# Performance work log

Hardware: AMD Instinct MI355X
Metric: run time of the kernel (lower is better)

Reference implementation:

```python
import jax, jax.numpy as jnp
import numpy as np

B, C, H, W = 4, 64, 64, 64
CI = C // 4  # inter_channels for q/k convs and SE fc


def setup_inputs() -> dict:
    key = jax.random.key(0)
    ks = jax.random.split(key, 12)
    s = lambda k, shape, fan: jax.random.normal(k, shape, jnp.float32) * (1.0 / np.sqrt(fan))
    return {
        "ftr": jax.random.normal(ks[0], (B, C, H, W), jnp.float32),
        "wq": s(ks[1], (CI, C), C), "bq": jnp.zeros((CI,), jnp.float32),
        "wk": s(ks[2], (CI, C), C), "bk": jnp.zeros((CI,), jnp.float32),
        "wv": s(ks[3], (C, C), C),  "bv": jnp.zeros((C,), jnp.float32),
        "delta": jnp.array([0.1], jnp.float32),
        "w_avg1": s(ks[4], (CI, C), C), "w_avg2": s(ks[5], (C, CI), CI),
        "w_max1": s(ks[6], (CI, C), C), "w_max2": s(ks[7], (C, CI), CI),
    }


def reference(ftr, wq, bq, wk, bk, wv, bv, delta, w_avg1, w_avg2, w_max1, w_max2):
    b, c, h, w = ftr.shape
    p = h * w
    x = ftr.reshape(b, c, p)                                   # [B,C,P]
    q = jnp.einsum('oc,bcp->bpo', wq, x) + bq                  # [B,P,CI]
    k = jnp.einsum('oc,bcp->bop', wk, x) + bk[:, None]         # [B,CI,P]
    v = jnp.einsum('oc,bcp->bop', wv, x) + bv[:, None]         # [B,C,P]
    scores = jnp.einsum('bpo,boq->bpq', q, k)                  # [B,P,P]
    weights = jax.nn.softmax(scores, axis=1)                   # softmax over dim=1 (queries), as in torch code
    G = jnp.einsum('bcp,bpq->bcq', v, weights).reshape(b, c, h, w)
    out = delta[0] * G + ftr
    # ChannelRecalibration (SE with avg+max pooling)
    f_avg = jnp.mean(out, axis=(2, 3))                         # [B,C]
    f_max = jnp.max(out, axis=(2, 3))                          # [B,C]
    a = jax.nn.relu(f_avg @ w_avg1.T) @ w_avg2.T
    m = jax.nn.relu(f_max @ w_max1.T) @ w_max2.T
    gate = jax.nn.sigmoid(a + m)[:, :, None, None]
    return gate * out
```

## Files before the change

### kernel.cpp

```cpp
#include <hip/hip_runtime.h>
#include <math.h>

#define PP 4096

typedef __attribute__((ext_vector_type(8))) short short8;
typedef __attribute__((ext_vector_type(4))) short short4v;
typedef __attribute__((ext_vector_type(4))) float float4v;

__device__ __forceinline__ short f2bf(float f) {
    union { float f; unsigned u; } v; v.f = f;
    unsigned r = v.u + 0x7FFFu + ((v.u >> 16) & 1u);
    return (short)(r >> 16);
}

#if __has_builtin(__builtin_amdgcn_mfma_f32_16x16x16bf16_1k)
__device__ __forceinline__ float4v mfma16(short4v a, short4v b, float4v c) {
    return __builtin_amdgcn_mfma_f32_16x16x16bf16_1k(a, b, c, 0, 0, 0);
}
#else
__device__ __forceinline__ float4v mfma16(short4v a, short4v b, float4v c) {
    short8 a8 = {a[0], a[1], a[2], a[3], 0, 0, 0, 0};
    short8 b8 = {b[0], b[1], b[2], b[3], 0, 0, 0, 0};
    return __builtin_amdgcn_mfma_f32_16x16x32_bf16(a8, b8, c, 0, 0, 0);
}
#endif

__global__ __launch_bounds__(256) void qkv_kernel(
    const float* __restrict__ ftr, const float* __restrict__ wq, const float* __restrict__ bq,
    const float* __restrict__ wk, const float* __restrict__ bk,
    const float* __restrict__ wv, const float* __restrict__ bv,
    short* __restrict__ q16, short* __restrict__ k16, short* __restrict__ v_a)
{
    __shared__ float xs[64][68] __attribute__((aligned(16)));
    __shared__ float wvs[64][68] __attribute__((aligned(16)));
    __shared__ float wq_t[64][20] __attribute__((aligned(16)));
    __shared__ float wk_t[64][20] __attribute__((aligned(16)));

    const int b  = blockIdx.x >> 6;
    const int p0 = (blockIdx.x & 63) << 6;
    const int tid = threadIdx.x;

    for (int idx = tid; idx < 1024; idx += 256) {
        int c = idx >> 4, j4 = (idx & 15) << 2;
        *(float4*)&xs[c][j4] = *(const float4*)(ftr + ((size_t)(b * 64 + c)) * PP + p0 + j4);
    }
    for (int idx = tid; idx < 1024; idx += 256) {
        int r = idx >> 4, j4 = (idx & 15) << 2;
        *(float4*)&wvs[r][j4] = *(const float4*)(wv + r * 64 + j4);
    }
    for (int idx = tid; idx < 1024; idx += 256) {
        int o = idx >> 6, c2 = idx & 63;
        wq_t[c2][o] = wq[idx];
        wk_t[c2][o] = wk[idx];
    }
    __syncthreads();

    {
        const int wg = tid >> 6, qd = (tid >> 4) & 3, cc = tid & 15;
        const int c = wg * 16 + cc;
        const float bvc = bv[c];
        #pragma unroll
        for (int kt = 0; kt < 2; ++kt) {
            const int col = kt * 32 + qd * 8;
            float a[8] = {0.f,0.f,0.f,0.f,0.f,0.f,0.f,0.f};
            #pragma unroll 8
            for (int c2 = 0; c2 < 64; ++c2) {
                float w = wvs[c][c2];
                float4 xa = *(const float4*)&xs[c2][col];
                float4 xb = *(const float4*)&xs[c2][col + 4];
                a[0] += w * xa.x; a[1] += w * xa.y; a[2] += w * xa.z; a[3] += w * xa.w;
                a[4] += w * xb.x; a[5] += w * xb.y; a[6] += w * xb.z; a[7] += w * xb.w;
            }
            const int ptg = ((p0 + kt * 32) >> 4) + (qd >> 1);
            const int qp0 = (qd & 1) * 2;
            #pragma unroll
            for (int h = 0; h < 2; ++h) {
                short4v pv;
                #pragma unroll
                for (int j = 0; j < 4; ++j) pv[j] = f2bf(a[h * 4 + j] + bvc);
                *(short4v*)(v_a + ((((size_t)(b * 256 + ptg)) * 4 + wg) * 64 + (qp0 + h) * 16 + cc) * 4) = pv;
            }
        }
    }

    {
        const int p_l = tid >> 2, sel = tid & 3;
        const int half = sel & 1, arr = sel >> 1;
        const float* Wtr = arr ? &wk_t[0][0] : &wq_t[0][0];
        float a[8] = {0.f,0.f,0.f,0.f,0.f,0.f,0.f,0.f};
        #pragma unroll 8
        for (int c2 = 0; c2 < 64; ++c2) {
            float x = xs[c2][p_l];
            float4 wA = *(const float4*)(Wtr + c2 * 20 + half * 8);
            float4 wB = *(const float4*)(Wtr + c2 * 20 + half * 8 + 4);
            a[0] += wA.x * x; a[1] += wA.y * x; a[2] += wA.z * x; a[3] += wA.w * x;
            a[4] += wB.x * x; a[5] += wB.y * x; a[6] += wB.z * x; a[7] += wB.w * x;
        }
        const float* bias = arr ? bk : bq;
        const float scl = arr ? 1.0f : 1.4426950408889634f;
        short8 pq;
        #pragma unroll
        for (int oo = 0; oo < 8; ++oo)
            pq[oo] = f2bf((a[oo] + bias[half * 8 + oo]) * scl);
        short* dst = (arr ? k16 : q16) + (((size_t)(b * PP + p0 + p_l)) << 4) + half * 8;
        *(short8*)dst = pq;
    }
}

__global__ __launch_bounds__(512, 2) void attn_kernel(
    const short* __restrict__ q16, const short* __restrict__ k16,
    const short* __restrict__ v_a,
    const float* __restrict__ ftr, const float* __restrict__ delta,
    float* __restrict__ out, float* __restrict__ psum, float* __restrict__ pmax)
{
    __shared__ float Obuf[8][16][66];
    __shared__ float lb[8][64];
    __shared__ float lfin[64];

    const int b    = blockIdx.x >> 6;
    const int qblk = blockIdx.x & 63;
    const int q0   = qblk << 6;
    const int tid  = threadIdx.x;
    const int lane = tid & 63;
    const int n    = lane & 15;
    const int quad = lane >> 4;
    const int ph   = tid >> 6;

    const float4v zf4 = {0.f, 0.f, 0.f, 0.f};
    const short4v ones = {0x3F80, 0x3F80, 0x3F80, 0x3F80};

    short4v bkf[4];
    #pragma unroll
    for (int nt = 0; nt < 4; ++nt)
        bkf[nt] = *(const short4v*)(k16 + ((size_t)(b * PP + q0 + nt * 16 + n) << 4) + quad * 4);

    const short* qrow = q16 + ((size_t)(b * PP + n) << 4) + quad * 4;
    const short* vrow = v_a + (size_t)b * 262144 + lane * 4;

    float4v acc[4][4], lacc[4];
    #pragma unroll
    for (int mt = 0; mt < 4; ++mt)
        #pragma unroll
        for (int nt = 0; nt < 4; ++nt) acc[mt][nt] = zf4;
    #pragma unroll
    for (int nt = 0; nt < 4; ++nt) lacc[nt] = zf4;

    const int pt0 = ph * 512;
    for (int it = 0; it < 8; ++it) {
        const int pt = pt0 + it * 64;
        const int pti = pt >> 4;

        short4v aq[4];
        #pragma unroll
        for (int f = 0; f < 4; ++f)
            aq[f] = *(const short4v*)(qrow + (size_t)(pt + f * 16) * 16);
        short4v va[4][4];
        #pragma unroll
        for (int f = 0; f < 4; ++f)
            #pragma unroll
            for (int mt = 0; mt < 4; ++mt)
                va[f][mt] = *(const short4v*)(vrow + (size_t)((pti + f) * 4 + mt) * 256);

        float4v sf_c[4], sf_n[4];
        #pragma unroll
        for (int nt = 0; nt < 4; ++nt)
            sf_c[nt] = mfma16(aq[0], bkf[nt], zf4);

        #pragma unroll
        for (int f = 0; f < 4; ++f) {
            if (f < 3) {
                #pragma unroll
                for (int nt = 0; nt < 4; ++nt)
                    sf_n[nt] = mfma16(aq[f + 1], bkf[nt], zf4);
            }
            short4v w[4];
            #pragma unroll
            for (int nt = 0; nt < 4; ++nt) {
                float w0 = __builtin_amdgcn_exp2f(sf_c[nt][0]);
                float w1 = __builtin_amdgcn_exp2f(sf_c[nt][1]);
                float w2 = __builtin_amdgcn_exp2f(sf_c[nt][2]);
                float w3 = __builtin_amdgcn_exp2f(sf_c[nt][3]);
                union { uint2 u; short4v s; } cv;
                cv.u.x = __builtin_amdgcn_perm(__float_as_uint(w1), __float_as_uint(w0), 0x07060302u);
                cv.u.y = __builtin_amdgcn_perm(__float_as_uint(w3), __float_as_uint(w2), 0x07060302u);
                w[nt] = cv.s;
            }
            #pragma unroll
            for (int nt = 0; nt < 4; ++nt)
                lacc[nt] = mfma16(ones, w[nt], lacc[nt]);
            #pragma unroll
            for (int mt = 0; mt < 4; ++mt)
                #pragma unroll
                for (int nt = 0; nt < 4; ++nt)
                    acc[mt][nt] = mfma16(va[f][mt], w[nt], acc[mt][nt]);
            #pragma unroll
            for (int nt = 0; nt < 4; ++nt) sf_c[nt] = sf_n[nt];
        }
    }

    if (quad == 0) {
        #pragma unroll
        for (int nt = 0; nt < 4; ++nt)
            lb[ph][nt * 16 + n] = lacc[nt][0];
    }
    __syncthreads();
    if (tid < 64) {
        float s = 0.f;
        #pragma unroll
        for (int p8 = 0; p8 < 8; ++p8) s += lb[p8][tid];
        lfin[tid] = delta[0] / s;
    }
    __syncthreads();

    const int c_l = tid >> 5;
    const int q2  = (tid & 31) * 2;
    #pragma unroll
    for (int mt = 0; mt < 4; ++mt) {
        #pragma unroll
        for (int nt = 0; nt < 4; ++nt)
            #pragma unroll
            for (int i = 0; i < 4; ++i)
                Obuf[ph][quad * 4 + i][nt * 16 + n] = acc[mt][nt][i];
        __syncthreads();
        const int c = mt * 16 + c_l;
        float o0 = 0.f, o1 = 0.f;
        #pragma unroll
        for (int p8 = 0; p8 < 8; ++p8) {
            o0 += Obuf[p8][c_l][q2];
            o1 += Obuf[p8][c_l][q2 + 1];
        }
        const size_t g = ((size_t)(b * 64 + c)) * PP + q0 + q2;
        float2 fv = *(const float2*)(ftr + g);
        o0 = o0 * lfin[q2]     + fv.x;
        o1 = o1 * lfin[q2 + 1] + fv.y;
        float2 ov; ov.x = o0; ov.y = o1;
        *(float2*)(out + g) = ov;
        float s = o0 + o1, m = fmaxf(o0, o1);
        s += __shfl_xor(s, 1); s += __shfl_xor(s, 2);
        s += __shfl_xor(s, 4); s += __shfl_xor(s, 8); s += __shfl_xor(s, 16);
        m = fmaxf(m, __shfl_xor(m, 1)); m = fmaxf(m, __shfl_xor(m, 2));
        m = fmaxf(m, __shfl_xor(m, 4)); m = fmaxf(m, __shfl_xor(m, 8));
        m = fmaxf(m, __shfl_xor(m, 16));
        if ((tid & 31) == 0) {
            psum[((size_t)(b * 64) + qblk) * 64 + c] = s;
            pmax[((size_t)(b * 64) + qblk) * 64 + c] = m;
        }
        __syncthreads();
    }
}

__global__ __launch_bounds__(256) void reduce_gate_kernel(
    const float* __restrict__ psum, const float* __restrict__ pmax,
    const float* __restrict__ w_avg1, const float* __restrict__ w_avg2,
    const float* __restrict__ w_max1, const float* __restrict__ w_max2,
    float* __restrict__ gate)
{
    const int b = blockIdx.x, t = threadIdx.x;
    const int c = t & 63, ch = t >> 6;
    float s = 0.f, m = -3.4e38f;
    for (int i = 0; i < 16; ++i) {
        const int qb = ch * 16 + i;
        s += psum[((size_t)(b * 64) + qb) * 64 + c];
        m = fmaxf(m, pmax[((size_t)(b * 64) + qb) * 64 + c]);
    }
    __shared__ float ss[4][64], sm[4][64], fa[64], fm[64], ha[16], hm[16];
    ss[ch][c] = s; sm[ch][c] = m;
    __syncthreads();
    if (t < 64) {
        fa[t] = (ss[0][t] + ss[1][t] + ss[2][t] + ss[3][t]) * (1.f / 4096.f);
        fm[t] = fmaxf(fmaxf(sm[0][t], sm[1][t]), fmaxf(sm[2][t], sm[3][t]));
    }
    __syncthreads();
    if (t < 16) {
        float a = 0.f;
        for (int cc = 0; cc < 64; ++cc) a += fa[cc] * w_avg1[t * 64 + cc];
        ha[t] = fmaxf(a, 0.f);
    } else if (t < 32) {
        float a = 0.f;
        for (int cc = 0; cc < 64; ++cc) a += fm[cc] * w_max1[(t - 16) * 64 + cc];
        hm[t - 16] = fmaxf(a, 0.f);
    }
    __syncthreads();
    if (t < 64) {
        float a = 0.f, mm = 0.f;
        #pragma unroll
        for (int i = 0; i < 16; ++i) {
            a  += ha[i] * w_avg2[t * 16 + i];
            mm += hm[i] * w_max2[t * 16 + i];
        }
        gate[b * 64 + t] = 1.f / (1.f + expf(-(a + mm)));
    }
}

__global__ __launch_bounds__(256) void mul_kernel(
    float* __restrict__ out, const float* __restrict__ gate)
{
    const float g = gate[blockIdx.x >> 2];
    const size_t e = ((size_t)blockIdx.x * 256 + threadIdx.x) * 4;
    float4 v = *(const float4*)(out + e);
    v.x *= g; v.y *= g; v.z *= g; v.w *= g;
    *(float4*)(out + e) = v;
}

extern "C" void kernel_launch(void* const* d_in, const int* in_sizes, int n_in,
                              void* d_out, int out_size, void* d_ws, size_t ws_size,
                              hipStream_t stream)
{
    const float* ftr    = (const float*)d_in[0];
    const float* wq     = (const float*)d_in[1];
    const float* bq     = (const float*)d_in[2];
    const float* wk     = (const float*)d_in[3];
    const float* bk     = (const float*)d_in[4];
    const float* wv     = (const float*)d_in[5];
    const float* bv     = (const float*)d_in[6];
    const float* delta  = (const float*)d_in[7];
    const float* w_avg1 = (const float*)d_in[8];
    const float* w_avg2 = (const float*)d_in[9];
    const float* w_max1 = (const float*)d_in[10];
    const float* w_max2 = (const float*)d_in[11];
    float* out = (float*)d_out;

    short* wsS  = (short*)d_ws;
    short* q16  = wsS;
    short* k16  = wsS + 262144;
    short* v_a  = wsS + 524288;
    float* fbase = (float*)(wsS + 1572864);
    float* psum = fbase;
    float* pmax = fbase + 16384;
    float* gate = fbase + 32768;

    qkv_kernel<<<256, 256, 0, stream>>>(ftr, wq, bq, wk, bk, wv, bv, q16, k16, v_a);
    attn_kernel<<<256, 512, 0, stream>>>(q16, k16, v_a, ftr, delta, out, psum, pmax);
    reduce_gate_kernel<<<4, 256, 0, stream>>>(psum, pmax, w_avg1, w_avg2, w_max1, w_max2, gate);
    mul_kernel<<<1024, 256, 0, stream>>>(out, gate);
}
```

Baseline: 129.0 us.

## Halve attention key tile to 32, double grid, replace ones-MFMA with scalar row sums

The attention and QKV kernels now each handle 32 columns per block instead of 64, so the grid doubles to 512 blocks and launch bounds allow 4 blocks per CU for better occupancy. The softmax denominator is now accumulated in scalar registers from the exp values and reduced with shuffles, instead of through extra MFMA calls with a ones vector. The QKV q/k projection splits the channel reduction across thread pairs and combines them with a shuffle. In exchange, each query/value fragment is reused over fewer key columns, which raises global and L2 traffic, and there are twice as many partial sums for the reduce kernel.

```diff
diff --git a/kernel.cpp b/kernel.cpp
--- a/kernel.cpp
+++ b/kernel.cpp
@@ -31,17 +31,17 @@
     const float* __restrict__ wv, const float* __restrict__ bv,
     short* __restrict__ q16, short* __restrict__ k16, short* __restrict__ v_a)
 {
-    __shared__ float xs[64][68] __attribute__((aligned(16)));
+    __shared__ float xs[64][36] __attribute__((aligned(16)));
     __shared__ float wvs[64][68] __attribute__((aligned(16)));
     __shared__ float wq_t[64][20] __attribute__((aligned(16)));
     __shared__ float wk_t[64][20] __attribute__((aligned(16)));
 
-    const int b  = blockIdx.x >> 6;
-    const int p0 = (blockIdx.x & 63) << 6;
+    const int b  = blockIdx.x >> 7;
+    const int p0 = (blockIdx.x & 127) << 5;
     const int tid = threadIdx.x;
 
-    for (int idx = tid; idx < 1024; idx += 256) {
-        int c = idx >> 4, j4 = (idx & 15) << 2;
+    for (int idx = tid; idx < 512; idx += 256) {
+        int c = idx >> 3, j4 = (idx & 7) << 2;
         *(float4*)&xs[c][j4] = *(const float4*)(ftr + ((size_t)(b * 64 + c)) * PP + p0 + j4);
     }
     for (int idx = tid; idx < 1024; idx += 256) {
@@ -59,67 +59,70 @@
         const int wg = tid >> 6, qd = (tid >> 4) & 3, cc = tid & 15;
         const int c = wg * 16 + cc;
         const float bvc = bv[c];
-        #pragma unroll
-        for (int kt = 0; kt < 2; ++kt) {
-            const int col = kt * 32 + qd * 8;
-            float a[8] = {0.f,0.f,0.f,0.f,0.f,0.f,0.f,0.f};
-            #pragma unroll 8
-            for (int c2 = 0; c2 < 64; ++c2) {
-                float w = wvs[c][c2];
-                float4 xa = *(const float4*)&xs[c2][col];
-                float4 xb = *(const float4*)&xs[c2][col + 4];
-                a[0] += w * xa.x; a[1] += w * xa.y; a[2] += w * xa.z; a[3] += w * xa.w;
-                a[4] += w * xb.x; a[5] += w * xb.y; a[6] += w * xb.z; a[7] += w * xb.w;
-            }
-            const int ptg = ((p0 + kt * 32) >> 4) + (qd >> 1);
-            const int qp0 = (qd & 1) * 2;
-            #pragma unroll
-            for (int h = 0; h < 2; ++h) {
-                short4v pv;
-                #pragma unroll
-                for (int j = 0; j < 4; ++j) pv[j] = f2bf(a[h * 4 + j] + bvc);
-                *(short4v*)(v_a + ((((size_t)(b * 256 + ptg)) * 4 + wg) * 64 + (qp0 + h) * 16 + cc) * 4) = pv;
-            }
-        }
-    }
-
-    {
-        const int p_l = tid >> 2, sel = tid & 3;
-        const int half = sel & 1, arr = sel >> 1;
-        const float* Wtr = arr ? &wk_t[0][0] : &wq_t[0][0];
+        const int col = qd * 8;
         float a[8] = {0.f,0.f,0.f,0.f,0.f,0.f,0.f,0.f};
         #pragma unroll 8
         for (int c2 = 0; c2 < 64; ++c2) {
+            float w = wvs[c][c2];
+            float4 xa = *(const float4*)&xs[c2][col];
+            float4 xb = *(const float4*)&xs[c2][col + 4];
+            a[0] += w * xa.x; a[1] += w * xa.y; a[2] += w * xa.z; a[3] += w * xa.w;
+            a[4] += w * xb.x; a[5] += w * xb.y; a[6] += w * xb.z; a[7] += w * xb.w;
+        }
+        const int ptg = (p0 >> 4) + (qd >> 1);
+        const int qp0 = (qd & 1) * 2;
+        #pragma unroll
+        for (int h = 0; h < 2; ++h) {
+            short4v pv;
+            #pragma unroll
+            for (int j = 0; j < 4; ++j) pv[j] = f2bf(a[h * 4 + j] + bvc);
+            *(short4v*)(v_a + ((((size_t)(b * 256 + ptg)) * 4 + wg) * 64 + (qp0 + h) * 16 + cc) * 4) = pv;
+        }
+    }
+
+    {
+        const int p_l = tid >> 3, sel = tid & 7;
+        const int ch = sel & 1, half = (sel >> 1) & 1, arr = sel >> 2;
+        const float* Wtr = arr ? &wk_t[0][0] : &wq_t[0][0];
+        float a[8] = {0.f,0.f,0.f,0.f,0.f,0.f,0.f,0.f};
+        const int c2lo = ch * 32;
+        #pragma unroll 8
+        for (int c2i = 0; c2i < 32; ++c2i) {
+            const int c2 = c2lo + c2i;
             float x = xs[c2][p_l];
             float4 wA = *(const float4*)(Wtr + c2 * 20 + half * 8);
             float4 wB = *(const float4*)(Wtr + c2 * 20 + half * 8 + 4);
             a[0] += wA.x * x; a[1] += wA.y * x; a[2] += wA.z * x; a[3] += wA.w * x;
             a[4] += wB.x * x; a[5] += wB.y * x; a[6] += wB.z * x; a[7] += wB.w * x;
         }
-        const float* bias = arr ? bk : bq;
-        const float scl = arr ? 1.0f : 1.4426950408889634f;
-        short8 pq;
-        #pragma unroll
-        for (int oo = 0; oo < 8; ++oo)
-            pq[oo] = f2bf((a[oo] + bias[half * 8 + oo]) * scl);
-        short* dst = (arr ? k16 : q16) + (((size_t)(b * PP + p0 + p_l)) << 4) + half * 8;
-        *(short8*)dst = pq;
-    }
-}
-
-__global__ __launch_bounds__(512, 2) void attn_kernel(
+        #pragma unroll
+        for (int oo = 0; oo < 8; ++oo) a[oo] += __shfl_xor(a[oo], 1);
+        if (ch == 0) {
+            const float* bias = arr ? bk : bq;
+            const float scl = arr ? 1.0f : 1.4426950408889634f;
+            short8 pq;
+            #pragma unroll
+            for (int oo = 0; oo < 8; ++oo)
+                pq[oo] = f2bf((a[oo] + bias[half * 8 + oo]) * scl);
+            short* dst = (arr ? k16 : q16) + (((size_t)(b * PP + p0 + p_l)) << 4) + half * 8;
+            *(short8*)dst = pq;
+        }
+    }
+}
+
+__global__ __launch_bounds__(512, 4) void attn_kernel(
     const short* __restrict__ q16, const short* __restrict__ k16,
     const short* __restrict__ v_a,
     const float* __restrict__ ftr, const float* __restrict__ delta,
     float* __restrict__ out, float* __restrict__ psum, float* __restrict__ pmax)
 {
-    __shared__ float Obuf[8][16][66];
-    __shared__ float lb[8][64];
-    __shared__ float lfin[64];
-
-    const int b    = blockIdx.x >> 6;
-    const int qblk = blockIdx.x & 63;
-    const int q0   = qblk << 6;
+    __shared__ float Obuf[8][16][34];
+    __shared__ float lb[8][32];
+    __shared__ float lfin[32];
+
+    const int b    = blockIdx.x >> 7;
+    const int qblk = blockIdx.x & 127;
+    const int q0   = qblk << 5;
     const int tid  = threadIdx.x;
     const int lane = tid & 63;
     const int n    = lane & 15;
@@ -127,25 +130,24 @@
     const int ph   = tid >> 6;
 
     const float4v zf4 = {0.f, 0.f, 0.f, 0.f};
-    const short4v ones = {0x3F80, 0x3F80, 0x3F80, 0x3F80};
-
-    short4v bkf[4];
+
+    short4v bkf[2];
     #pragma unroll
-    for (int nt = 0; nt < 4; ++nt)
+    for (int nt = 0; nt < 2; ++nt)
         bkf[nt] = *(const short4v*)(k16 + ((size_t)(b * PP + q0 + nt * 16 + n) << 4) + quad * 4);
 
     const short* qrow = q16 + ((size_t)(b * PP + n) << 4) + quad * 4;
     const short* vrow = v_a + (size_t)b * 262144 + lane * 4;
 
-    float4v acc[4][4], lacc[4];
+    float4v acc[4][2];
     #pragma unroll
     for (int mt = 0; mt < 4; ++mt)
         #pragma unroll
-        for (int nt = 0; nt < 4; ++nt) acc[mt][nt] = zf4;
-    #pragma unroll
-    for (int nt = 0; nt < 4; ++nt) lacc[nt] = zf4;
+        for (int nt = 0; nt < 2; ++nt) acc[mt][nt] = zf4;
+    float lsum[2] = {0.f, 0.f};
 
     const int pt0 = ph * 512;
+    #pragma unroll 2
     for (int it = 0; it < 8; ++it) {
         const int pt = pt0 + it * 64;
         const int pti = pt >> 4;
@@ -161,50 +163,49 @@
             for (int mt = 0; mt < 4; ++mt)
                 va[f][mt] = *(const short4v*)(vrow + (size_t)((pti + f) * 4 + mt) * 256);
 
-        float4v sf_c[4], sf_n[4];
-        #pragma unroll
-        for (int nt = 0; nt < 4; ++nt)
+        float4v sf_c[2], sf_n[2];
+        #pragma unroll
+        for (int nt = 0; nt < 2; ++nt)
             sf_c[nt] = mfma16(aq[0], bkf[nt], zf4);
 
         #pragma unroll
         for (int f = 0; f < 4; ++f) {
             if (f < 3) {
                 #pragma unroll
-                for (int nt = 0; nt < 4; ++nt)
+                for (int nt = 0; nt < 2; ++nt)
                     sf_n[nt] = mfma16(aq[f + 1], bkf[nt], zf4);
             }
-            short4v w[4];
-            #pragma unroll
-            for (int nt = 0; nt < 4; ++nt) {
+            short4v w[2];
+            #pragma unroll
+            for (int nt = 0; nt < 2; ++nt) {
                 float w0 = __builtin_amdgcn_exp2f(sf_c[nt][0]);
                 float w1 = __builtin_amdgcn_exp2f(sf_c[nt][1]);
                 float w2 = __builtin_amdgcn_exp2f(sf_c[nt][2]);
                 float w3 = __builtin_amdgcn_exp2f(sf_c[nt][3]);
+                lsum[nt] += (w0 + w1) + (w2 + w3);
                 union { uint2 u; short4v s; } cv;
                 cv.u.x = __builtin_amdgcn_perm(__float_as_uint(w1), __float_as_uint(w0), 0x07060302u);
                 cv.u.y = __builtin_amdgcn_perm(__float_as_uint(w3), __float_as_uint(w2), 0x07060302u);
                 w[nt] = cv.s;
             }
             #pragma unroll
-            for (int nt = 0; nt < 4; ++nt)
-                lacc[nt] = mfma16(ones, w[nt], lacc[nt]);
-            #pragma unroll
             for (int mt = 0; mt < 4; ++mt)
                 #pragma unroll
-                for (int nt = 0; nt < 4; ++nt)
+                for (int nt = 0; nt < 2; ++nt)
                     acc[mt][nt] = mfma16(va[f][mt], w[nt], acc[mt][nt]);
             #pragma unroll
-            for (int nt = 0; nt < 4; ++nt) sf_c[nt] = sf_n[nt];
-        }
-    }
-
+            for (int nt = 0; nt < 2; ++nt) sf_c[nt] = sf_n[nt];
+        }
+    }
+
+    lsum[0] += __shfl_xor(lsum[0], 16); lsum[0] += __shfl_xor(lsum[0], 32);
+    lsum[1] += __shfl_xor(lsum[1], 16); lsum[1] += __shfl_xor(lsum[1], 32);
     if (quad == 0) {
-        #pragma unroll
-        for (int nt = 0; nt < 4; ++nt)
-            lb[ph][nt * 16 + n] = lacc[nt][0];
-    }
-    __syncthreads();
-    if (tid < 64) {
+        lb[ph][n]      = lsum[0];
+        lb[ph][16 + n] = lsum[1];
+    }
+    __syncthreads();
+    if (tid < 32) {
         float s = 0.f;
         #pragma unroll
         for (int p8 = 0; p8 < 8; ++p8) s += lb[p8][tid];
@@ -213,37 +214,31 @@
     __syncthreads();
 
     const int c_l = tid >> 5;
-    const int q2  = (tid & 31) * 2;
+    const int q   = tid & 31;
     #pragma unroll
     for (int mt = 0; mt < 4; ++mt) {
         #pragma unroll
-        for (int nt = 0; nt < 4; ++nt)
+        for (int nt = 0; nt < 2; ++nt)
             #pragma unroll
             for (int i = 0; i < 4; ++i)
                 Obuf[ph][quad * 4 + i][nt * 16 + n] = acc[mt][nt][i];
         __syncthreads();
         const int c = mt * 16 + c_l;
-        float o0 = 0.f, o1 = 0.f;
-        #pragma unroll
-        for (int p8 = 0; p8 < 8; ++p8) {
-            o0 += Obuf[p8][c_l][q2];
-            o1 += Obuf[p8][c_l][q2 + 1];
-        }
-        const size_t g = ((size_t)(b * 64 + c)) * PP + q0 + q2;
-        float2 fv = *(const float2*)(ftr + g);
-        o0 = o0 * lfin[q2]     + fv.x;
-        o1 = o1 * lfin[q2 + 1] + fv.y;
-        float2 ov; ov.x = o0; ov.y = o1;
-        *(float2*)(out + g) = ov;
-        float s = o0 + o1, m = fmaxf(o0, o1);
+        float o = 0.f;
+        #pragma unroll
+        for (int p8 = 0; p8 < 8; ++p8) o += Obuf[p8][c_l][q];
+        const size_t g = ((size_t)(b * 64 + c)) * PP + q0 + q;
+        o = o * lfin[q] + ftr[g];
+        out[g] = o;
+        float s = o, m = o;
         s += __shfl_xor(s, 1); s += __shfl_xor(s, 2);
         s += __shfl_xor(s, 4); s += __shfl_xor(s, 8); s += __shfl_xor(s, 16);
         m = fmaxf(m, __shfl_xor(m, 1)); m = fmaxf(m, __shfl_xor(m, 2));
         m = fmaxf(m, __shfl_xor(m, 4)); m = fmaxf(m, __shfl_xor(m, 8));
         m = fmaxf(m, __shfl_xor(m, 16));
-        if ((tid & 31) == 0) {
-            psum[((size_t)(b * 64) + qblk) * 64 + c] = s;
-            pmax[((size_t)(b * 64) + qblk) * 64 + c] = m;
+        if (q == 0) {
+            psum[((size_t)(b * 128) + qblk) * 64 + c] = s;
+            pmax[((size_t)(b * 128) + qblk) * 64 + c] = m;
         }
         __syncthreads();
     }
@@ -258,10 +253,10 @@
     const int b = blockIdx.x, t = threadIdx.x;
     const int c = t & 63, ch = t >> 6;
     float s = 0.f, m = -3.4e38f;
-    for (int i = 0; i < 16; ++i) {
-        const int qb = ch * 16 + i;
-        s += psum[((size_t)(b * 64) + qb) * 64 + c];
-        m = fmaxf(m, pmax[((size_t)(b * 64) + qb) * 64 + c]);
+    for (int i = 0; i < 32; ++i) {
+        const int qb = ch * 32 + i;
+        s += psum[((size_t)(b * 128) + qb) * 64 + c];
+        m = fmaxf(m, pmax[((size_t)(b * 128) + qb) * 64 + c]);
     }
     __shared__ float ss[4][64], sm[4][64], fa[64], fm[64], ha[16], hm[16];
     ss[ch][c] = s; sm[ch][c] = m;
@@ -326,11 +321,11 @@
     short* v_a  = wsS + 524288;
     float* fbase = (float*)(wsS + 1572864);
     float* psum = fbase;
-    float* pmax = fbase + 16384;
-    float* gate = fbase + 32768;
-
-    qkv_kernel<<<256, 256, 0, stream>>>(ftr, wq, bq, wk, bk, wv, bv, q16, k16, v_a);
-    attn_kernel<<<256, 512, 0, stream>>>(q16, k16, v_a, ftr, delta, out, psum, pmax);
+    float* pmax = fbase + 32768;
+    float* gate = fbase + 65536;
+
+    qkv_kernel<<<512, 256, 0, stream>>>(ftr, wq, bq, wk, bk, wv, bv, q16, k16, v_a);
+    attn_kernel<<<512, 512, 0, stream>>>(q16, k16, v_a, ftr, delta, out, psum, pmax);
     reduce_gate_kernel<<<4, 256, 0, stream>>>(psum, pmax, w_avg1, w_avg2, w_max1, w_max2, gate);
     mul_kernel<<<1024, 256, 0, stream>>>(out, gate);
 }
```

After: 128.5 us. About the same (-0.4%).
